# Optimization experiments

Measured on AMD Instinct MI355X. Metric: run time of the kernel, lower is better.

The kernel has to match this reference:

```python
import jax, jax.numpy as jnp
import numpy as np

D_LATENTS = 256
B, N = 8, 4096
EPS = 1e-5  # BatchNorm eps (torch default)


def _w(k, shape):
    return jax.random.normal(k, shape, jnp.float32) * 0.05


def setup_inputs() -> dict:
    key = jax.random.key(0)
    ks = jax.random.split(key, 20)
    d4, d2, d = D_LATENTS // 4, D_LATENTS // 2, D_LATENTS
    def bn(k):
        k1, k2 = jax.random.split(k)
        g = 1.0 + 0.1 * jax.random.normal(k1, (0,), jnp.float32)  # placeholder
        return g
    inp = {
        "x": jax.random.normal(ks[0], (B, 3, N), jnp.float32),
        "conv1_w": _w(ks[1], (d4, 3)),
        "bn1_g": 1.0 + 0.1 * jax.random.normal(ks[2], (d4,), jnp.float32),
        "bn1_b": 0.1 * jax.random.normal(ks[3], (d4,), jnp.float32),
        "conv2_w": _w(ks[4], (d4, d4)),
        "bn2_g": 1.0 + 0.1 * jax.random.normal(ks[5], (d4,), jnp.float32),
        "bn2_b": 0.1 * jax.random.normal(ks[6], (d4,), jnp.float32),
        "le0_w1": _w(ks[7], (d2, d2)),
        "le0_g1": 1.0 + 0.1 * jax.random.normal(ks[8], (d2,), jnp.float32),
        "le0_b1": 0.1 * jax.random.normal(ks[9], (d2,), jnp.float32),
        "le0_w2": _w(ks[10], (d2, d2)),
        "le0_g2": 1.0 + 0.1 * jax.random.normal(ks[11], (d2,), jnp.float32),
        "le0_b2": 0.1 * jax.random.normal(ks[12], (d2,), jnp.float32),
        "le1_w1": _w(ks[13], (d, d)),
        "le1_g1": 1.0 + 0.1 * jax.random.normal(ks[14], (d,), jnp.float32),
        "le1_b1": 0.1 * jax.random.normal(ks[15], (d,), jnp.float32),
        "le1_w2": _w(ks[16], (d, d)),
        "le1_g2": 1.0 + 0.1 * jax.random.normal(ks[17], (d,), jnp.float32),
        "le1_b2": 0.1 * jax.random.normal(ks[18], (d,), jnp.float32),
    }
    return inp


def _bn_relu(y, g, b, axes, ch_axis):
    # BatchNorm (training-mode batch stats, biased var like torch) + ReLU
    m = jnp.mean(y, axes, keepdims=True)
    v = jnp.var(y, axes, keepdims=True)
    shp = [1] * y.ndim
    shp[ch_axis] = -1
    return jax.nn.relu((y - m) * jax.lax.rsqrt(v + EPS) * g.reshape(shp) + b.reshape(shp))


def _square_distance(src, dst):
    # src [B,S,3], dst [B,N,3] -> [B,S,N]
    return (jnp.sum(src * src, -1, keepdims=True)
            - 2.0 * jnp.einsum('bsc,bnc->bsn', src, dst)
            + jnp.sum(dst * dst, -1)[:, None, :])


def _fps(xyz, npoint):
    # farthest point sampling, deterministic start at index 0
    Bb, Nn, _ = xyz.shape
    def step(carry, _):
        dist_min, farthest = carry
        centroid = jnp.take_along_axis(xyz, farthest[:, None, None], axis=1)  # [B,1,3]
        d = jnp.sum((xyz - centroid) ** 2, -1)  # [B,N]
        dist_min = jnp.minimum(dist_min, d)
        nxt = jnp.argmax(dist_min, -1).astype(jnp.int32)
        return (dist_min, nxt), farthest
    init = (jnp.full((Bb, Nn), 1e10, xyz.dtype), jnp.zeros((Bb,), jnp.int32))
    _, idxs = jax.lax.scan(step, init, None, length=npoint)
    return jnp.transpose(idxs)  # [B, npoint]


def _sample_and_group(npoint, nsample, xyz, points):
    # PCT-style: FPS centers, kNN neighbors (radius unused), concat(rel, center)
    Bb = xyz.shape[0]
    fps_idx = _fps(xyz, npoint)                       # [B,S]
    bidx = jnp.arange(Bb)[:, None]
    new_xyz = xyz[bidx, fps_idx]                      # [B,S,3]
    new_pts = points[bidx, fps_idx]                   # [B,S,D]
    d2 = _square_distance(new_xyz, xyz)               # [B,S,N]
    _, knn_idx = jax.lax.top_k(-d2, nsample)          # [B,S,ns]
    grouped = points[jnp.arange(Bb)[:, None, None], knn_idx]  # [B,S,ns,D]
    center = new_pts[:, :, None, :]
    feat = jnp.concatenate([grouped - center,
                            jnp.broadcast_to(center, grouped.shape)], axis=-1)
    return new_xyz, feat  # [B,S,3], [B,S,ns,2D]


def _local_encoder(x4, w1, g1, b1, w2, g2, b2):
    # x4: [b,n,s,d] -> conv1x1/bn/relu x2 over channel dim, max over s -> [b,out,n]
    y = jnp.einsum('bnsd,od->bnos', x4, w1)
    y = _bn_relu(y, g1, b1, (0, 1, 3), 2)
    y = jnp.einsum('bnis,oi->bnos', y, w2)
    y = _bn_relu(y, g2, b2, (0, 1, 3), 2)
    y = jnp.max(y, axis=3)                # [b,n,out]
    return jnp.transpose(y, (0, 2, 1))    # [b,out,n]


def reference(x, conv1_w, bn1_g, bn1_b, conv2_w, bn2_g, bn2_b,
              le0_w1, le0_g1, le0_b1, le0_w2, le0_g2, le0_b2,
              le1_w1, le1_g1, le1_b1, le1_w2, le1_g2, le1_b2):
    xyz = jnp.transpose(x, (0, 2, 1))                 # [B,N,3]
    y = jnp.einsum('bcn,oc->bon', x, conv1_w)
    y = _bn_relu(y, bn1_g, bn1_b, (0, 2), 1)
    y = jnp.einsum('bcn,oc->bon', y, conv2_w)
    y = _bn_relu(y, bn2_g, bn2_b, (0, 2), 1)
    pts = jnp.transpose(y, (0, 2, 1))                 # [B,N,d4]
    new_xyz, feat = _sample_and_group(512, 32, xyz, pts)       # [B,512,32,d2]
    f0 = _local_encoder(feat, le0_w1, le0_g1, le0_b1, le0_w2, le0_g2, le0_b2)  # [B,d2,512]
    pts1 = jnp.transpose(f0, (0, 2, 1))
    _, feat2 = _sample_and_group(256, 32, new_xyz, pts1)       # [B,256,32,d]
    f1 = _local_encoder(feat2, le1_w1, le1_g1, le1_b1, le1_w2, le1_g2, le1_b2)  # [B,d,256]
    return f1
```

## Files before the change

kernel.cpp:

```cpp
#include <hip/hip_runtime.h>

constexpr int B_  = 8;
constexpr int N_  = 4096;
constexpr int NP1 = 512;
constexpr int NP2 = 256;
constexpr float EPS_ = 1e-5f;

typedef __attribute__((ext_vector_type(8))) short bhalf8;
typedef __attribute__((ext_vector_type(4))) float f32x4;

__device__ inline short f2bf(float f) {
  union { float fv; unsigned u; } v; v.fv = f;
  unsigned r = v.u + 0x7FFFu + ((v.u >> 16) & 1u);
  return (short)(r >> 16);
}

template<int CTRL>
__device__ inline void dpp_amax(unsigned &khi, unsigned &klo) {
  unsigned ohi = (unsigned)__builtin_amdgcn_mov_dpp((int)khi, CTRL, 0xF, 0xF, false);
  unsigned olo = (unsigned)__builtin_amdgcn_mov_dpp((int)klo, CTRL, 0xF, 0xF, false);
  if (ohi > khi || (ohi == khi && olo > klo)) { khi = ohi; klo = olo; }
}
__device__ inline void swz16_amax(unsigned &khi, unsigned &klo) {
  unsigned ohi = (unsigned)__builtin_amdgcn_ds_swizzle((int)khi, 0x401F);
  unsigned olo = (unsigned)__builtin_amdgcn_ds_swizzle((int)klo, 0x401F);
  if (ohi > khi || (ohi == khi && olo > klo)) { khi = ohi; klo = olo; }
}
__device__ inline void x32_amax(unsigned &khi, unsigned &klo) {
  unsigned ohi = (unsigned)__shfl_xor((int)khi, 32);
  unsigned olo = (unsigned)__shfl_xor((int)klo, 32);
  if (ohi > khi || (ohi == khi && olo > klo)) { khi = ohi; klo = olo; }
}
__device__ inline unsigned ford(float f) {
  unsigned u = __float_as_uint(f);
  return u ^ (((unsigned)((int)u >> 31)) | 0x80000000u);
}

constexpr int S_BN1 = 0;
constexpr int S_BN2 = 128;
constexpr int S_L0A = 256;
constexpr int S_L0B = 512;
constexpr int S_L1A = 768;
constexpr int S_L1B = 1280;
constexpr int S_TOTAL = 1792;

constexpr size_t OFF_T1   = 0;
constexpr size_t OFF_YBUF = OFF_T1   + 2097152;
constexpr size_t OFF_PTS1 = OFF_YBUF + 16777216;
constexpr size_t OFF_NXYZ = OFF_PTS1 + 524288;
constexpr size_t OFF_WT2C = OFF_NXYZ + 12288;
constexpr size_t OFF_BW0A = OFF_WT2C + 4096;
constexpr size_t OFF_BW0B = OFF_BW0A + 8192;
constexpr size_t OFF_BW1A = OFF_BW0B + 8192;
constexpr size_t OFF_BW1B = OFF_BW1A + 32768;
constexpr size_t OFF_STAT = OFF_BW1B + 32768;
constexpr size_t OFF_INT  = OFF_STAT + 1792;

__global__ void prep_kernel(const float* __restrict__ conv2w,
                            const float* __restrict__ w0a, const float* __restrict__ w0b,
                            const float* __restrict__ w1a, const float* __restrict__ w1b,
                            float* __restrict__ wt2c,
                            short* __restrict__ b0a, short* __restrict__ b0b,
                            short* __restrict__ b1a, short* __restrict__ b1b) {
  int idx = blockIdx.x * 256 + threadIdx.x;
  if (idx < 4096) { int d = idx >> 6, o = idx & 63; wt2c[idx] = conv2w[o*64 + d]; return; }
  idx -= 4096;
  const float* w; short* dst; int D;
  if      (idx <  2048) { w = w0a; dst = b0a; D = 128; }
  else if (idx <  4096) { w = w0b; dst = b0b; D = 128; idx -= 2048; }
  else if (idx < 12288) { w = w1a; dst = b1a; D = 256; idx -= 4096; }
  else if (idx < 20480) { w = w1b; dst = b1b; D = 256; idx -= 12288; }
  else return;
  int kblk = idx / D, o = idx % D;
  const float* src = w + (size_t)o*D + kblk*8;
  bhalf8 pk;
#pragma unroll
  for (int j = 0; j < 8; ++j) pk[j] = f2bf(src[j]);
  *(bhalf8*)&dst[(size_t)idx*8] = pk;
}

__global__ __launch_bounds__(256) void conv1_kernel(
    const float* __restrict__ x, const float* __restrict__ w,
    float* __restrict__ t1, float* __restrict__ stats) {
  __shared__ float xs[3][64];
  __shared__ float redS[4][64], redQ[4][64];
  int blk = blockIdx.x;
  int b = blk >> 6, n0 = (blk & 63) << 6;
  int t = threadIdx.x;
  if (t < 192) { int c = t >> 6, nl = t & 63; xs[c][nl] = x[((size_t)b*3 + c)*N_ + n0 + nl]; }
  __syncthreads();
  int o = t & 63, ng = t >> 6;
  float w0 = w[o*3+0], w1 = w[o*3+1], w2 = w[o*3+2];
  float ls = 0.f, lq = 0.f;
#pragma unroll
  for (int k = 0; k < 16; ++k) {
    int nl = ng*16 + k;
    float y = xs[0][nl]*w0 + xs[1][nl]*w1 + xs[2][nl]*w2;
    t1[((size_t)b*N_ + n0 + nl)*64 + o] = y;
    ls += y; lq += y*y;
  }
  redS[ng][o] = ls; redQ[ng][o] = lq;
  __syncthreads();
  if (t < 64) {
    float s = redS[0][t]+redS[1][t]+redS[2][t]+redS[3][t];
    float q = redQ[0][t]+redQ[1][t]+redQ[2][t]+redQ[3][t];
    atomicAdd(&stats[S_BN1 + t], s);
    atomicAdd(&stats[S_BN1 + 64 + t], q);
  }
}

__global__ __launch_bounds__(256) void conv2_kernel(
    const float* __restrict__ t1, const float* __restrict__ g1, const float* __restrict__ b1,
    const float* __restrict__ wt2c, float* __restrict__ t2, float* __restrict__ stats) {
  constexpr int P = 68;
  __shared__ float at[64*P];
  __shared__ float sc[64], sh[64];
  __shared__ float redS[4][64], redQ[4][64];
  int blk = blockIdx.x;
  int b = blk >> 6, n0 = (blk & 63) << 6;
  int t = threadIdx.x;
  if (t < 64) {
    float m = stats[S_BN1 + t] * (1.f/32768.f);
    float v = stats[S_BN1 + 64 + t] * (1.f/32768.f) - m*m;
    float s = g1[t] * rsqrtf(v + EPS_);
    sc[t] = s; sh[t] = b1[t] - m*s;
  }
  __syncthreads();
  for (int e = t; e < 4096; e += 256) {
    int nl = e >> 6, c = e & 63;
    float v = t1[((size_t)b*N_ + n0 + nl)*64 + c];
    at[c*P + nl] = fmaxf(v*sc[c] + sh[c], 0.f);
  }
  __syncthreads();
  int o = t & 63, ng = t >> 6;
  float acc[16];
#pragma unroll
  for (int k = 0; k < 16; ++k) acc[k] = 0.f;
  for (int i = 0; i < 64; ++i) {
    float wv = wt2c[i*64 + o];
    const float* ar = &at[i*P + ng*16];
#pragma unroll
    for (int k = 0; k < 16; k += 4) {
      float4 a4 = *(const float4*)(ar + k);
      acc[k+0] += a4.x*wv; acc[k+1] += a4.y*wv;
      acc[k+2] += a4.z*wv; acc[k+3] += a4.w*wv;
    }
  }
  float ls = 0.f, lq = 0.f;
#pragma unroll
  for (int k = 0; k < 16; ++k) {
    float y = acc[k];
    t2[((size_t)b*N_ + n0 + ng*16 + k)*64 + o] = y;
    ls += y; lq += y*y;
  }
  redS[ng][o] = ls; redQ[ng][o] = lq;
  __syncthreads();
  if (t < 64) {
    float s = redS[0][t]+redS[1][t]+redS[2][t]+redS[3][t];
    float q = redQ[0][t]+redQ[1][t]+redQ[2][t]+redQ[3][t];
    atomicAdd(&stats[S_BN2 + t], s);
    atomicAdd(&stats[S_BN2 + 64 + t], q);
  }
}

__global__ __launch_bounds__(256) void bn2fin_kernel(
    const float* __restrict__ t2, const float* __restrict__ g2, const float* __restrict__ b2,
    const float* __restrict__ stats, float* __restrict__ pts) {
  int idx = blockIdx.x*256 + threadIdx.x;
  int o = idx & 63;
  float m = stats[S_BN2 + o] * (1.f/32768.f);
  float v = stats[S_BN2 + 64 + o] * (1.f/32768.f) - m*m;
  float s = g2[o] * rsqrtf(v + EPS_);
  pts[idx] = fmaxf(t2[idx]*s + (b2[o] - m*s), 0.f);
}

template<int NPTS, int NSEL1, int NSEL2, int NT>
__global__ __launch_bounds__(NT) void fps_fused_kernel(
    const float* __restrict__ x,
    int* __restrict__ sel1, float* __restrict__ nxyz, int* __restrict__ sel2) {
  constexpr int K  = NPTS / NT;
  constexpr int NS = NT / 32;
  __shared__ float lx[NPTS], ly[NPTS], lz[NPTS];
  __shared__ float sx[NSEL1], sy[NSEL1], sz[NSEL1];
  __shared__ unsigned long long wk[2][NS];
  __shared__ int seli1[NSEL1];
  __shared__ int seli2[NSEL2];
  int b = blockIdx.x, t = threadIdx.x;
  int lane = t & 63, wid = t >> 6;
  const float* cb = x + (size_t)b * 3 * NPTS;
  for (int i = t; i < NPTS; i += NT) {
    lx[i] = cb[i]; ly[i] = cb[NPTS + i]; lz[i] = cb[2*NPTS + i];
  }
  __syncthreads();
  float px[K], py[K], pz[K], dm[K];
#pragma unroll
  for (int k = 0; k < K; ++k) {
    int p = t + k*NT;
    px[k] = lx[p]; py[k] = ly[p]; pz[k] = lz[p];
    dm[k] = 1e10f;
  }
  float cx = lx[0], cy = ly[0], cz = lz[0];
  if (t == 0) { seli1[0] = 0; sx[0] = cx; sy[0] = cy; sz[0] = cz; }
  for (int it = 1; it < NSEL1; ++it) {
    float bv = -1.f; int bi = 0;
#pragma unroll
    for (int k = 0; k < K; ++k) {
      float dx = px[k]-cx, dy = py[k]-cy, dz = pz[k]-cz;
      float d = dx*dx + dy*dy + dz*dz;
      float nd = fminf(dm[k], d);
      dm[k] = nd;
      if (nd > bv) { bv = nd; bi = t + k*NT; }
    }
    unsigned khi = __float_as_uint(bv), klo = ~(unsigned)bi;
    dpp_amax<0xB1>(khi, klo);
    dpp_amax<0x4E>(khi, klo);
    dpp_amax<0x141>(khi, klo);
    dpp_amax<0x140>(khi, klo);
    swz16_amax(khi, klo);
    int p = it & 1;
    if ((lane & 31) == 0)
      wk[p][wid*2 + (lane >> 5)] = ((unsigned long long)khi << 32) | klo;
    __syncthreads();
    unsigned long long best = wk[p][0];
#pragma unroll
    for (int i2 = 1; i2 < NS; ++i2) { unsigned long long v2 = wk[p][i2]; if (v2 > best) best = v2; }
    int Bi = (int)(~(unsigned)best);
    cx = lx[Bi]; cy = ly[Bi]; cz = lz[Bi];
    if (t == 0) { seli1[it] = Bi; sx[it] = cx; sy[it] = cy; sz[it] = cz; }
  }
  __syncthreads();
  if (t < 64) {
    constexpr int K2 = NSEL1 / 64;
    float qx[K2], qy[K2], qz[K2], dm2[K2];
#pragma unroll
    for (int k = 0; k < K2; ++k) {
      int p = t + k*64;
      qx[k] = sx[p]; qy[k] = sy[p]; qz[k] = sz[p];
      dm2[k] = 1e10f;
    }
    cx = sx[0]; cy = sy[0]; cz = sz[0];
    if (t == 0) seli2[0] = 0;
    for (int it = 1; it < NSEL2; ++it) {
      float bv = -1.f; int bi = 0;
#pragma unroll
      for (int k = 0; k < K2; ++k) {
        float dx = qx[k]-cx, dy = qy[k]-cy, dz = qz[k]-cz;
        float d = dx*dx + dy*dy + dz*dz;
        float nd = fminf(dm2[k], d);
        dm2[k] = nd;
        if (nd > bv) { bv = nd; bi = t + k*64; }
      }
      unsigned khi = __float_as_uint(bv), klo = ~(unsigned)bi;
      dpp_amax<0xB1>(khi, klo);
      dpp_amax<0x4E>(khi, klo);
      dpp_amax<0x141>(khi, klo);
      dpp_amax<0x140>(khi, klo);
      swz16_amax(khi, klo);
      x32_amax(khi, klo);
      int Bi = (int)~klo;
      cx = sx[Bi]; cy = sy[Bi]; cz = sz[Bi];
      if (t == 0) seli2[it] = Bi;
    }
  } else {
    for (int i = t - 64; i < NSEL1; i += NT - 64) {
      sel1[(size_t)b*NSEL1 + i] = seli1[i];
      float* q = nxyz + ((size_t)b*NSEL1 + i)*3;
      q[0] = sx[i]; q[1] = sy[i]; q[2] = sz[i];
    }
  }
  __syncthreads();
  for (int i = t; i < NSEL2; i += NT) sel2[(size_t)b*NSEL2 + i] = seli2[i];
}

template<int NDST, int NQ, int NT, bool XLAY>
__global__ __launch_bounds__(NT) void knn_kernel(
    const float* __restrict__ dst, const float* __restrict__ nxyz,
    const int* __restrict__ qmap, int* __restrict__ knn_out) {
  constexpr int K  = NDST / NT;
  constexpr int NS = NT / 32;
  __shared__ unsigned long long wk[2][NS];
  __shared__ int kos[32];
  int blk = blockIdx.x, t = threadIdx.x;
  int b = blk / NQ, q = blk % NQ;
  int qrow = b*NP1 + (qmap ? qmap[b*NQ + q] : q);
  float qx = nxyz[qrow*3+0], qy = nxyz[qrow*3+1], qz = nxyz[qrow*3+2];
  float q2 = (qx*qx + qy*qy) + qz*qz;
  const float* db = dst + (size_t)b * (XLAY ? 3*NDST : NDST*3);
  float d2r[K];
#pragma unroll
  for (int k = 0; k < K; ++k) {
    int j = t + k*NT;
    float xx, yy, zz;
    if (XLAY) { xx = db[j]; yy = db[NDST + j]; zz = db[2*NDST + j]; }
    else      { xx = db[j*3]; yy = db[j*3+1]; zz = db[j*3+2]; }
    float dot = (qx*xx + qy*yy) + qz*zz;
    float p2  = (xx*xx + yy*yy) + zz*zz;
    d2r[k] = (q2 - 2.f*dot) + p2;
  }
  for (int r = 0; r < 32; ++r) {
    float bv = 3e38f; int bi = t;
#pragma unroll
    for (int k = 0; k < K; ++k) {
      float v = d2r[k];
      if (v < bv) { bv = v; bi = t + k*NT; }
    }
    unsigned khi = ~ford(bv), klo = ~(unsigned)bi;
    dpp_amax<0xB1>(khi, klo);
    dpp_amax<0x4E>(khi, klo);
    dpp_amax<0x141>(khi, klo);
    dpp_amax<0x140>(khi, klo);
    swz16_amax(khi, klo);
    int p = r & 1;
    if ((t & 31) == 0)
      wk[p][t >> 5] = ((unsigned long long)khi << 32) | klo;
    __syncthreads();
    unsigned long long best = wk[p][0];
#pragma unroll
    for (int i2 = 1; i2 < NS; ++i2) { unsigned long long v2 = wk[p][i2]; if (v2 > best) best = v2; }
    int Bi = (int)(~(unsigned)best);
    if (t == 0) kos[r] = Bi;
#pragma unroll
    for (int k = 0; k < K; ++k)
      if (t + k*NT == Bi) d2r[k] = 3e38f;
  }
  __syncthreads();
  if (t < 32) knn_out[((size_t)b*NQ + q)*32 + t] = kos[t];
}

template<int D, int PW, int NP, int SRCN, int SOFF>
__global__ __launch_bounds__(256) void gemm1_kernel(
    const float* __restrict__ pts, const int* __restrict__ knn,
    const int* __restrict__ cent, const short* __restrict__ bw,
    float* __restrict__ ybuf, float* __restrict__ stats) {
  constexpr int KB = D/8;
  __shared__ __align__(16) short As[64*D];
  __shared__ float cen_s[2*PW];
  __shared__ int kid_s[64];
  __shared__ float sstat[2*D];
  int t = threadIdx.x, blk = blockIdx.x;
  int g0 = blk*2;
  if (t < 64) {
    int grp = t >> 5, s = t & 31;
    kid_s[t] = knn[((size_t)(g0+grp))*32 + s];
  }
  for (int i = t; i < 2*PW; i += 256) {
    int grp = i / PW, d = i % PW;
    int g = g0 + grp; int b = g / NP; int ci = cent[g];
    cen_s[i] = pts[((size_t)b*SRCN + ci)*PW + d];
  }
  for (int i = t; i < 2*D; i += 256) sstat[i] = 0.f;
  __syncthreads();
  for (int task = t; task < 64*KB; task += 256) {
    int row = task / KB, c = task % KB;
    int grp = row >> 5;
    int g = g0 + grp; int b = g / NP;
    int d = c*8;
    float v0,v1,v2,v3,v4,v5,v6,v7;
    if (d < PW) {
      const float* src = pts + ((size_t)b*SRCN + kid_s[row])*PW + d;
      float4 x0 = *(const float4*)src, x1 = *(const float4*)(src+4);
      const float* cc = &cen_s[grp*PW + d];
      v0=x0.x-cc[0]; v1=x0.y-cc[1]; v2=x0.z-cc[2]; v3=x0.w-cc[3];
      v4=x1.x-cc[4]; v5=x1.y-cc[5]; v6=x1.z-cc[6]; v7=x1.w-cc[7];
    } else {
      const float* cc = &cen_s[grp*PW + d - PW];
      v0=cc[0]; v1=cc[1]; v2=cc[2]; v3=cc[3]; v4=cc[4]; v5=cc[5]; v6=cc[6]; v7=cc[7];
    }
    bhalf8 pk;
    pk[0]=f2bf(v0); pk[1]=f2bf(v1); pk[2]=f2bf(v2); pk[3]=f2bf(v3);
    pk[4]=f2bf(v4); pk[5]=f2bf(v5); pk[6]=f2bf(v6); pk[7]=f2bf(v7);
    int a16 = row*KB + (c ^ (row & 7));
    *(bhalf8*)&As[a16*8] = pk;
  }
  __syncthreads();
  int w = t >> 6, l = t & 63, lr = l & 15, lg = l >> 4;
  f32x4 acc[D/16];
#pragma unroll
  for (int ct = 0; ct < D/16; ++ct) acc[ct] = (f32x4){0.f,0.f,0.f,0.f};
  int r = w*16 + lr;
#pragma unroll
  for (int kg = 0; kg < D/32; ++kg) {
    int c = (kg*4 + lg) ^ (r & 7);
    bhalf8 af = *(const bhalf8*)&As[(r*KB + c)*8];
#pragma unroll
    for (int ct = 0; ct < D/16; ++ct) {
      bhalf8 bf = *(const bhalf8*)&bw[((size_t)(kg*4 + lg)*D + ct*16 + lr)*8];
      acc[ct] = __builtin_amdgcn_mfma_f32_16x16x32_bf16(af, bf, acc[ct], 0, 0, 0);
    }
  }
  size_t rb = (size_t)blk*64 + w*16 + lg*4;
#pragma unroll
  for (int ct = 0; ct < D/16; ++ct) {
    int col = ct*16 + lr;
    f32x4 a = acc[ct];
    float* yp = ybuf + rb*D + col;
    yp[0] = a[0]; yp[(size_t)D] = a[1]; yp[(size_t)2*D] = a[2]; yp[(size_t)3*D] = a[3];
    float s = a[0]+a[1]+a[2]+a[3];
    float q = a[0]*a[0]+a[1]*a[1]+a[2]*a[2]+a[3]*a[3];
    s += __shfl_xor(s, 16); q += __shfl_xor(q, 16);
    s += __shfl_xor(s, 32); q += __shfl_xor(q, 32);
    if (lg == 0) { atomicAdd(&sstat[col], s); atomicAdd(&sstat[D+col], q); }
  }
  __syncthreads();
  for (int i = t; i < 2*D; i += 256) atomicAdd(&stats[SOFF+i], sstat[i]);
}

template<int D, int SIN, int SOUT, int CNT>
__global__ __launch_bounds__(256) void gemm2_kernel(
    const float* __restrict__ g1, const float* __restrict__ b1,
    const short* __restrict__ bw, const float* __restrict__ ybuf,
    float* __restrict__ mm, float* __restrict__ stats) {
  __shared__ __align__(16) float scsh[2*D];
  __shared__ float sstat[2*D];
  __shared__ float wmax[4][D], wmin[4][D];
  int t = threadIdx.x, blk = blockIdx.x;
  for (int i = t; i < D; i += 256) {
    float m = stats[SIN + i] * (1.f/(float)CNT);
    float v = stats[SIN + D + i] * (1.f/(float)CNT) - m*m;
    float s = g1[i] * rsqrtf(v + EPS_);
    scsh[i] = s; scsh[D+i] = b1[i] - m*s;
  }
  for (int i = t; i < 2*D; i += 256) sstat[i] = 0.f;
  __syncthreads();
  int w = t >> 6, l = t & 63, lr = l & 15, lg = l >> 4;
  size_t row = (size_t)blk*64 + w*16 + lr;
  const float* yrow = ybuf + row*D;
  f32x4 acc[D/16];
#pragma unroll
  for (int ct = 0; ct < D/16; ++ct) acc[ct] = (f32x4){0.f,0.f,0.f,0.f};
#pragma unroll
  for (int kg = 0; kg < D/32; ++kg) {
    int k = kg*32 + lg*8;
    float4 y0 = *(const float4*)(yrow + k);
    float4 y1 = *(const float4*)(yrow + k + 4);
    bhalf8 af;
    af[0] = f2bf(fmaxf(y0.x*scsh[k+0] + scsh[D+k+0], 0.f));
    af[1] = f2bf(fmaxf(y0.y*scsh[k+1] + scsh[D+k+1], 0.f));
    af[2] = f2bf(fmaxf(y0.z*scsh[k+2] + scsh[D+k+2], 0.f));
    af[3] = f2bf(fmaxf(y0.w*scsh[k+3] + scsh[D+k+3], 0.f));
    af[4] = f2bf(fmaxf(y1.x*scsh[k+4] + scsh[D+k+4], 0.f));
    af[5] = f2bf(fmaxf(y1.y*scsh[k+5] + scsh[D+k+5], 0.f));
    af[6] = f2bf(fmaxf(y1.z*scsh[k+6] + scsh[D+k+6], 0.f));
    af[7] = f2bf(fmaxf(y1.w*scsh[k+7] + scsh[D+k+7], 0.f));
#pragma unroll
    for (int ct = 0; ct < D/16; ++ct) {
      bhalf8 bf = *(const bhalf8*)&bw[((size_t)(kg*4 + lg)*D + ct*16 + lr)*8];
      acc[ct] = __builtin_amdgcn_mfma_f32_16x16x32_bf16(af, bf, acc[ct], 0, 0, 0);
    }
  }
#pragma unroll
  for (int ct = 0; ct < D/16; ++ct) {
    int col = ct*16 + lr;
    f32x4 a = acc[ct];
    float mx = fmaxf(fmaxf(a[0], a[1]), fmaxf(a[2], a[3]));
    float mn = fminf(fminf(a[0], a[1]), fminf(a[2], a[3]));
    mx = fmaxf(mx, __shfl_xor(mx, 16)); mn = fminf(mn, __shfl_xor(mn, 16));
    mx = fmaxf(mx, __shfl_xor(mx, 32)); mn = fminf(mn, __shfl_xor(mn, 32));
    if (lg == 0) { wmax[w][col] = mx; wmin[w][col] = mn; }
    float s = a[0]+a[1]+a[2]+a[3];
    float q = a[0]*a[0]+a[1]*a[1]+a[2]*a[2]+a[3]*a[3];
    s += __shfl_xor(s, 16); q += __shfl_xor(q, 16);
    s += __shfl_xor(s, 32); q += __shfl_xor(q, 32);
    if (lg == 0) { atomicAdd(&sstat[col], s); atomicAdd(&sstat[D+col], q); }
  }
  __syncthreads();
  for (int i = t; i < 2*D; i += 256) {
    int g = i / D, col = i - g*D;
    float mx = fmaxf(wmax[2*g][col], wmax[2*g+1][col]);
    float mn = fminf(wmin[2*g][col], wmin[2*g+1][col]);
    float* mp = mm + ((size_t)blk*2 + g)*2*D;
    mp[col] = mx; mp[D + col] = mn;
    atomicAdd(&stats[SOUT+i], sstat[i]);
  }
}

template<int D, int NP, int SOFF, int CNT, bool TR>
__global__ __launch_bounds__(256) void le3_kernel(
    const float* __restrict__ g2, const float* __restrict__ b2,
    const float* __restrict__ mm, const float* __restrict__ stats,
    float* __restrict__ out) {
  int idx = blockIdx.x*256 + threadIdx.x;
  int g = idx / D, o = idx - g*D;
  float m = stats[SOFF + o] * (1.f/(float)CNT);
  float v = stats[SOFF + D + o] * (1.f/(float)CNT) - m*m;
  float s = g2[o] * rsqrtf(v + EPS_);
  float sh = b2[o] - m*s;
  const float* mp = mm + (size_t)g*2*D;
  float pick = (s >= 0.f) ? mp[o] : mp[D + o];
  float r = fmaxf(pick*s + sh, 0.f);
  if (TR) { int b = g / NP, n = g - b*NP; out[((size_t)b*D + o)*NP + n] = r; }
  else    out[(size_t)g*D + o] = r;
}

extern "C" void kernel_launch(void* const* d_in, const int* in_sizes, int n_in,
                              void* d_out, int out_size, void* d_ws, size_t ws_size,
                              hipStream_t stream) {
  (void)in_sizes; (void)n_in; (void)out_size; (void)ws_size;
  const float* x       = (const float*)d_in[0];
  const float* conv1_w = (const float*)d_in[1];
  const float* bn1_g   = (const float*)d_in[2];
  const float* bn1_b   = (const float*)d_in[3];
  const float* conv2_w = (const float*)d_in[4];
  const float* bn2_g   = (const float*)d_in[5];
  const float* bn2_b   = (const float*)d_in[6];
  const float* le0_w1  = (const float*)d_in[7];
  const float* le0_g1  = (const float*)d_in[8];
  const float* le0_b1  = (const float*)d_in[9];
  const float* le0_w2  = (const float*)d_in[10];
  const float* le0_g2  = (const float*)d_in[11];
  const float* le0_b2  = (const float*)d_in[12];
  const float* le1_w1  = (const float*)d_in[13];
  const float* le1_g1  = (const float*)d_in[14];
  const float* le1_b1  = (const float*)d_in[15];
  const float* le1_w2  = (const float*)d_in[16];
  const float* le1_g2  = (const float*)d_in[17];
  const float* le1_b2  = (const float*)d_in[18];

  float* ws   = (float*)d_ws;
  float* t1   = ws + OFF_T1;
  float* ybuf = ws + OFF_YBUF;
  float* t2   = ybuf;
  float* mm   = t1;
  float* pts1 = ws + OFF_PTS1;
  float* nxyz = ws + OFF_NXYZ;
  float* wt2c = ws + OFF_WT2C;
  short* bw0a = (short*)(ws + OFF_BW0A);
  short* bw0b = (short*)(ws + OFF_BW0B);
  short* bw1a = (short*)(ws + OFF_BW1A);
  short* bw1b = (short*)(ws + OFF_BW1B);
  float* stats = ws + OFF_STAT;
  int* fps1 = (int*)(ws + OFF_INT);
  int* fps2 = fps1 + 4096;
  int* knn1 = fps2 + 2048;
  int* knn2 = knn1 + 131072;

  hipMemsetAsync(stats, 0, S_TOTAL*sizeof(float), stream);
  prep_kernel<<<96, 256, 0, stream>>>(conv2_w, le0_w1, le0_w2, le1_w1, le1_w2,
                                      wt2c, bw0a, bw0b, bw1a, bw1b);
  conv1_kernel<<<512, 256, 0, stream>>>(x, conv1_w, t1, stats);
  conv2_kernel<<<512, 256, 0, stream>>>(t1, bn1_g, bn1_b, wt2c, t2, stats);
  bn2fin_kernel<<<8192, 256, 0, stream>>>(t2, bn2_g, bn2_b, stats, t1);

  fps_fused_kernel<4096, 512, 256, 256><<<8, 256, 0, stream>>>(x, fps1, nxyz, fps2);
  knn_kernel<4096, 512, 256, true ><<<4096, 256, 0, stream>>>(x, nxyz, nullptr, knn1);
  knn_kernel< 512, 256, 256, false><<<2048, 256, 0, stream>>>(nxyz, nxyz, fps2, knn2);

  gemm1_kernel<128,  64, 512, 4096, S_L0A><<<2048, 256, 0, stream>>>(t1, knn1, fps1, bw0a, ybuf, stats);
  gemm2_kernel<128, S_L0A, S_L0B, 131072><<<2048, 256, 0, stream>>>(le0_g1, le0_b1, bw0b, ybuf, mm, stats);
  le3_kernel<128, 512, S_L0B, 131072, false><<<2048, 256, 0, stream>>>(le0_g2, le0_b2, mm, stats, pts1);

  gemm1_kernel<256, 128, 256,  512, S_L1A><<<1024, 256, 0, stream>>>(pts1, knn2, fps2, bw1a, ybuf, stats);
  gemm2_kernel<256, S_L1A, S_L1B, 65536><<<1024, 256, 0, stream>>>(le1_g1, le1_b1, bw1b, ybuf, mm, stats);
  le3_kernel<256, 256, S_L1B, 65536, true><<<2048, 256, 0, stream>>>(le1_g2, le1_b2, mm, stats, (float*)d_out);
}
```

Measured before the change: 1.020 ms.

## Fuse weight prep, conv/BN front end and FPS into one persistent kernel

Weight preparation, conv1, conv2, the BN2 finalize and farthest point sampling become a single launch of 264 blocks. The first 8 blocks run FPS, one per batch. The other 256 blocks process the conv tiles and sync between the BN stages with atomic-counter grid barriers. This removes four kernel launches and lets the serial FPS work run alongside the conv/BN pipeline instead of after it. In exchange it depends on all blocks being co-resident for the spin barriers, and it makes every block reserve the larger FPS shared-memory footprint.

After: 973.0 us. 1.05x faster.

```diff
diff --git a/kernel.cpp b/kernel.cpp
--- a/kernel.cpp
+++ b/kernel.cpp
@@ -54,23 +54,22 @@
 constexpr size_t OFF_BW1A = OFF_BW0B + 8192;
 constexpr size_t OFF_BW1B = OFF_BW1A + 32768;
 constexpr size_t OFF_STAT = OFF_BW1B + 32768;
-constexpr size_t OFF_INT  = OFF_STAT + 1792;
-
-__global__ void prep_kernel(const float* __restrict__ conv2w,
-                            const float* __restrict__ w0a, const float* __restrict__ w0b,
-                            const float* __restrict__ w1a, const float* __restrict__ w1b,
-                            float* __restrict__ wt2c,
-                            short* __restrict__ b0a, short* __restrict__ b0b,
-                            short* __restrict__ b1a, short* __restrict__ b1b) {
-  int idx = blockIdx.x * 256 + threadIdx.x;
+constexpr size_t OFF_CNT  = OFF_STAT + S_TOTAL;
+constexpr size_t OFF_INT  = OFF_CNT + 16;
+
+__device__ inline void prep_elem(int idx, const float* __restrict__ conv2w,
+                                 const float* __restrict__ w0a, const float* __restrict__ w0b,
+                                 const float* __restrict__ w1a, const float* __restrict__ w1b,
+                                 float* __restrict__ wt2c,
+                                 short* __restrict__ b0a, short* __restrict__ b0b,
+                                 short* __restrict__ b1a, short* __restrict__ b1b) {
   if (idx < 4096) { int d = idx >> 6, o = idx & 63; wt2c[idx] = conv2w[o*64 + d]; return; }
   idx -= 4096;
   const float* w; short* dst; int D;
   if      (idx <  2048) { w = w0a; dst = b0a; D = 128; }
   else if (idx <  4096) { w = w0b; dst = b0b; D = 128; idx -= 2048; }
   else if (idx < 12288) { w = w1a; dst = b1a; D = 256; idx -= 4096; }
-  else if (idx < 20480) { w = w1b; dst = b1b; D = 256; idx -= 12288; }
-  else return;
+  else                  { w = w1b; dst = b1b; D = 256; idx -= 12288; }
   int kblk = idx / D, o = idx % D;
   const float* src = w + (size_t)o*D + kblk*8;
   bhalf8 pk;
@@ -79,176 +78,63 @@
   *(bhalf8*)&dst[(size_t)idx*8] = pk;
 }
 
-__global__ __launch_bounds__(256) void conv1_kernel(
-    const float* __restrict__ x, const float* __restrict__ w,
-    float* __restrict__ t1, float* __restrict__ stats) {
-  __shared__ float xs[3][64];
-  __shared__ float redS[4][64], redQ[4][64];
-  int blk = blockIdx.x;
-  int b = blk >> 6, n0 = (blk & 63) << 6;
+struct FpsSmem {
+  float lx[4096], ly[4096], lz[4096];
+  float sx[512], sy[512], sz[512];
+  unsigned long long wk[2][8];
+  int seli1[512];
+  int seli2[256];
+};
+struct ConvSmem {
+  float xs[3][64];
+  float redS[4][64], redQ[4][64];
+  float sc[64], sh[64];
+  float at[64*68];
+};
+
+__global__ __launch_bounds__(256) void front_kernel(
+    const float* __restrict__ x,
+    const float* __restrict__ conv1w, const float* __restrict__ bn1g, const float* __restrict__ bn1b,
+    const float* __restrict__ conv2w, const float* __restrict__ bn2g, const float* __restrict__ bn2b,
+    const float* __restrict__ w0a, const float* __restrict__ w0b,
+    const float* __restrict__ w1a, const float* __restrict__ w1b,
+    float* __restrict__ wt2c,
+    short* __restrict__ b0a, short* __restrict__ b0b,
+    short* __restrict__ b1a, short* __restrict__ b1b,
+    float* __restrict__ t1, float* __restrict__ t2,
+    float* __restrict__ stats, int* __restrict__ cnt,
+    int* __restrict__ sel1, float* __restrict__ nxyz, int* __restrict__ sel2) {
+  __shared__ __align__(16) char smem_raw[sizeof(FpsSmem)];
   int t = threadIdx.x;
-  if (t < 192) { int c = t >> 6, nl = t & 63; xs[c][nl] = x[((size_t)b*3 + c)*N_ + n0 + nl]; }
-  __syncthreads();
-  int o = t & 63, ng = t >> 6;
-  float w0 = w[o*3+0], w1 = w[o*3+1], w2 = w[o*3+2];
-  float ls = 0.f, lq = 0.f;
-#pragma unroll
-  for (int k = 0; k < 16; ++k) {
-    int nl = ng*16 + k;
-    float y = xs[0][nl]*w0 + xs[1][nl]*w1 + xs[2][nl]*w2;
-    t1[((size_t)b*N_ + n0 + nl)*64 + o] = y;
-    ls += y; lq += y*y;
-  }
-  redS[ng][o] = ls; redQ[ng][o] = lq;
-  __syncthreads();
-  if (t < 64) {
-    float s = redS[0][t]+redS[1][t]+redS[2][t]+redS[3][t];
-    float q = redQ[0][t]+redQ[1][t]+redQ[2][t]+redQ[3][t];
-    atomicAdd(&stats[S_BN1 + t], s);
-    atomicAdd(&stats[S_BN1 + 64 + t], q);
-  }
-}
-
-__global__ __launch_bounds__(256) void conv2_kernel(
-    const float* __restrict__ t1, const float* __restrict__ g1, const float* __restrict__ b1,
-    const float* __restrict__ wt2c, float* __restrict__ t2, float* __restrict__ stats) {
-  constexpr int P = 68;
-  __shared__ float at[64*P];
-  __shared__ float sc[64], sh[64];
-  __shared__ float redS[4][64], redQ[4][64];
-  int blk = blockIdx.x;
-  int b = blk >> 6, n0 = (blk & 63) << 6;
-  int t = threadIdx.x;
-  if (t < 64) {
-    float m = stats[S_BN1 + t] * (1.f/32768.f);
-    float v = stats[S_BN1 + 64 + t] * (1.f/32768.f) - m*m;
-    float s = g1[t] * rsqrtf(v + EPS_);
-    sc[t] = s; sh[t] = b1[t] - m*s;
-  }
-  __syncthreads();
-  for (int e = t; e < 4096; e += 256) {
-    int nl = e >> 6, c = e & 63;
-    float v = t1[((size_t)b*N_ + n0 + nl)*64 + c];
-    at[c*P + nl] = fmaxf(v*sc[c] + sh[c], 0.f);
-  }
-  __syncthreads();
-  int o = t & 63, ng = t >> 6;
-  float acc[16];
-#pragma unroll
-  for (int k = 0; k < 16; ++k) acc[k] = 0.f;
-  for (int i = 0; i < 64; ++i) {
-    float wv = wt2c[i*64 + o];
-    const float* ar = &at[i*P + ng*16];
-#pragma unroll
-    for (int k = 0; k < 16; k += 4) {
-      float4 a4 = *(const float4*)(ar + k);
-      acc[k+0] += a4.x*wv; acc[k+1] += a4.y*wv;
-      acc[k+2] += a4.z*wv; acc[k+3] += a4.w*wv;
-    }
-  }
-  float ls = 0.f, lq = 0.f;
-#pragma unroll
-  for (int k = 0; k < 16; ++k) {
-    float y = acc[k];
-    t2[((size_t)b*N_ + n0 + ng*16 + k)*64 + o] = y;
-    ls += y; lq += y*y;
-  }
-  redS[ng][o] = ls; redQ[ng][o] = lq;
-  __syncthreads();
-  if (t < 64) {
-    float s = redS[0][t]+redS[1][t]+redS[2][t]+redS[3][t];
-    float q = redQ[0][t]+redQ[1][t]+redQ[2][t]+redQ[3][t];
-    atomicAdd(&stats[S_BN2 + t], s);
-    atomicAdd(&stats[S_BN2 + 64 + t], q);
-  }
-}
-
-__global__ __launch_bounds__(256) void bn2fin_kernel(
-    const float* __restrict__ t2, const float* __restrict__ g2, const float* __restrict__ b2,
-    const float* __restrict__ stats, float* __restrict__ pts) {
-  int idx = blockIdx.x*256 + threadIdx.x;
-  int o = idx & 63;
-  float m = stats[S_BN2 + o] * (1.f/32768.f);
-  float v = stats[S_BN2 + 64 + o] * (1.f/32768.f) - m*m;
-  float s = g2[o] * rsqrtf(v + EPS_);
-  pts[idx] = fmaxf(t2[idx]*s + (b2[o] - m*s), 0.f);
-}
-
-template<int NPTS, int NSEL1, int NSEL2, int NT>
-__global__ __launch_bounds__(NT) void fps_fused_kernel(
-    const float* __restrict__ x,
-    int* __restrict__ sel1, float* __restrict__ nxyz, int* __restrict__ sel2) {
-  constexpr int K  = NPTS / NT;
-  constexpr int NS = NT / 32;
-  __shared__ float lx[NPTS], ly[NPTS], lz[NPTS];
-  __shared__ float sx[NSEL1], sy[NSEL1], sz[NSEL1];
-  __shared__ unsigned long long wk[2][NS];
-  __shared__ int seli1[NSEL1];
-  __shared__ int seli2[NSEL2];
-  int b = blockIdx.x, t = threadIdx.x;
-  int lane = t & 63, wid = t >> 6;
-  const float* cb = x + (size_t)b * 3 * NPTS;
-  for (int i = t; i < NPTS; i += NT) {
-    lx[i] = cb[i]; ly[i] = cb[NPTS + i]; lz[i] = cb[2*NPTS + i];
-  }
-  __syncthreads();
-  float px[K], py[K], pz[K], dm[K];
-#pragma unroll
-  for (int k = 0; k < K; ++k) {
-    int p = t + k*NT;
-    px[k] = lx[p]; py[k] = ly[p]; pz[k] = lz[p];
-    dm[k] = 1e10f;
-  }
-  float cx = lx[0], cy = ly[0], cz = lz[0];
-  if (t == 0) { seli1[0] = 0; sx[0] = cx; sy[0] = cy; sz[0] = cz; }
-  for (int it = 1; it < NSEL1; ++it) {
-    float bv = -1.f; int bi = 0;
+  if (blockIdx.x < 8) {
+    constexpr int NPTS = 4096, NSEL1 = 512, NSEL2 = 256, NT = 256;
+    constexpr int K = NPTS / NT, NS = NT / 32;
+    FpsSmem& S = *reinterpret_cast<FpsSmem*>(smem_raw);
+    int b = blockIdx.x;
+    int lane = t & 63, wid = t >> 6;
+    const float* cb = x + (size_t)b * 3 * NPTS;
+    for (int i = t; i < NPTS; i += NT) {
+      S.lx[i] = cb[i]; S.ly[i] = cb[NPTS + i]; S.lz[i] = cb[2*NPTS + i];
+    }
+    __syncthreads();
+    float px[K], py[K], pz[K], dm[K];
 #pragma unroll
     for (int k = 0; k < K; ++k) {
-      float dx = px[k]-cx, dy = py[k]-cy, dz = pz[k]-cz;
-      float d = dx*dx + dy*dy + dz*dz;
-      float nd = fminf(dm[k], d);
-      dm[k] = nd;
-      if (nd > bv) { bv = nd; bi = t + k*NT; }
-    }
-    unsigned khi = __float_as_uint(bv), klo = ~(unsigned)bi;
-    dpp_amax<0xB1>(khi, klo);
-    dpp_amax<0x4E>(khi, klo);
-    dpp_amax<0x141>(khi, klo);
-    dpp_amax<0x140>(khi, klo);
-    swz16_amax(khi, klo);
-    int p = it & 1;
-    if ((lane & 31) == 0)
-      wk[p][wid*2 + (lane >> 5)] = ((unsigned long long)khi << 32) | klo;
-    __syncthreads();
-    unsigned long long best = wk[p][0];
-#pragma unroll
-    for (int i2 = 1; i2 < NS; ++i2) { unsigned long long v2 = wk[p][i2]; if (v2 > best) best = v2; }
-    int Bi = (int)(~(unsigned)best);
-    cx = lx[Bi]; cy = ly[Bi]; cz = lz[Bi];
-    if (t == 0) { seli1[it] = Bi; sx[it] = cx; sy[it] = cy; sz[it] = cz; }
-  }
-  __syncthreads();
-  if (t < 64) {
-    constexpr int K2 = NSEL1 / 64;
-    float qx[K2], qy[K2], qz[K2], dm2[K2];
-#pragma unroll
-    for (int k = 0; k < K2; ++k) {
-      int p = t + k*64;
-      qx[k] = sx[p]; qy[k] = sy[p]; qz[k] = sz[p];
-      dm2[k] = 1e10f;
-    }
-    cx = sx[0]; cy = sy[0]; cz = sz[0];
-    if (t == 0) seli2[0] = 0;
-    for (int it = 1; it < NSEL2; ++it) {
+      int p = t + k*NT;
+      px[k] = S.lx[p]; py[k] = S.ly[p]; pz[k] = S.lz[p];
+      dm[k] = 1e10f;
+    }
+    float cx = S.lx[0], cy = S.ly[0], cz = S.lz[0];
+    if (t == 0) { S.seli1[0] = 0; S.sx[0] = cx; S.sy[0] = cy; S.sz[0] = cz; }
+    for (int it = 1; it < NSEL1; ++it) {
       float bv = -1.f; int bi = 0;
 #pragma unroll
-      for (int k = 0; k < K2; ++k) {
-        float dx = qx[k]-cx, dy = qy[k]-cy, dz = qz[k]-cz;
+      for (int k = 0; k < K; ++k) {
+        float dx = px[k]-cx, dy = py[k]-cy, dz = pz[k]-cz;
         float d = dx*dx + dy*dy + dz*dz;
-        float nd = fminf(dm2[k], d);
-        dm2[k] = nd;
-        if (nd > bv) { bv = nd; bi = t + k*64; }
+        float nd = fminf(dm[k], d);
+        dm[k] = nd;
+        if (nd > bv) { bv = nd; bi = t + k*NT; }
       }
       unsigned khi = __float_as_uint(bv), klo = ~(unsigned)bi;
       dpp_amax<0xB1>(khi, klo);
@@ -256,20 +142,165 @@
       dpp_amax<0x141>(khi, klo);
       dpp_amax<0x140>(khi, klo);
       swz16_amax(khi, klo);
-      x32_amax(khi, klo);
-      int Bi = (int)~klo;
-      cx = sx[Bi]; cy = sy[Bi]; cz = sz[Bi];
-      if (t == 0) seli2[it] = Bi;
-    }
-  } else {
-    for (int i = t - 64; i < NSEL1; i += NT - 64) {
-      sel1[(size_t)b*NSEL1 + i] = seli1[i];
-      float* q = nxyz + ((size_t)b*NSEL1 + i)*3;
-      q[0] = sx[i]; q[1] = sy[i]; q[2] = sz[i];
-    }
-  }
-  __syncthreads();
-  for (int i = t; i < NSEL2; i += NT) sel2[(size_t)b*NSEL2 + i] = seli2[i];
+      int p = it & 1;
+      if ((lane & 31) == 0)
+        S.wk[p][wid*2 + (lane >> 5)] = ((unsigned long long)khi << 32) | klo;
+      __syncthreads();
+      unsigned long long best = S.wk[p][0];
+#pragma unroll
+      for (int i2 = 1; i2 < NS; ++i2) { unsigned long long v2 = S.wk[p][i2]; if (v2 > best) best = v2; }
+      int Bi = (int)(~(unsigned)best);
+      cx = S.lx[Bi]; cy = S.ly[Bi]; cz = S.lz[Bi];
+      if (t == 0) { S.seli1[it] = Bi; S.sx[it] = cx; S.sy[it] = cy; S.sz[it] = cz; }
+    }
+    __syncthreads();
+    if (t < 64) {
+      constexpr int K2 = NSEL1 / 64;
+      float qx[K2], qy[K2], qz[K2], dm2[K2];
+#pragma unroll
+      for (int k = 0; k < K2; ++k) {
+        int p = t + k*64;
+        qx[k] = S.sx[p]; qy[k] = S.sy[p]; qz[k] = S.sz[p];
+        dm2[k] = 1e10f;
+      }
+      cx = S.sx[0]; cy = S.sy[0]; cz = S.sz[0];
+      if (t == 0) S.seli2[0] = 0;
+      for (int it = 1; it < NSEL2; ++it) {
+        float bv = -1.f; int bi = 0;
+#pragma unroll
+        for (int k = 0; k < K2; ++k) {
+          float dx = qx[k]-cx, dy = qy[k]-cy, dz = qz[k]-cz;
+          float d = dx*dx + dy*dy + dz*dz;
+          float nd = fminf(dm2[k], d);
+          dm2[k] = nd;
+          if (nd > bv) { bv = nd; bi = t + k*64; }
+        }
+        unsigned khi = __float_as_uint(bv), klo = ~(unsigned)bi;
+        dpp_amax<0xB1>(khi, klo);
+        dpp_amax<0x4E>(khi, klo);
+        dpp_amax<0x141>(khi, klo);
+        dpp_amax<0x140>(khi, klo);
+        swz16_amax(khi, klo);
+        x32_amax(khi, klo);
+        int Bi = (int)~klo;
+        cx = S.sx[Bi]; cy = S.sy[Bi]; cz = S.sz[Bi];
+        if (t == 0) S.seli2[it] = Bi;
+      }
+    } else {
+      for (int i = t - 64; i < NSEL1; i += NT - 64) {
+        sel1[(size_t)b*NSEL1 + i] = S.seli1[i];
+        float* q = nxyz + ((size_t)b*NSEL1 + i)*3;
+        q[0] = S.sx[i]; q[1] = S.sy[i]; q[2] = S.sz[i];
+      }
+    }
+    __syncthreads();
+    for (int i = t; i < NSEL2; i += NT) sel2[(size_t)b*NSEL2 + i] = S.seli2[i];
+    return;
+  }
+  ConvSmem& C = *reinterpret_cast<ConvSmem*>(smem_raw);
+  int cb = blockIdx.x - 8;
+  { int idx = cb*256 + t;
+    if (idx < 24576) prep_elem(idx, conv2w, w0a, w0b, w1a, w1b, wt2c, b0a, b0b, b1a, b1b); }
+  for (int tile = cb; tile < 512; tile += 256) {
+    int b = tile >> 6, n0 = (tile & 63) << 6;
+    if (t < 192) { int c = t >> 6, nl = t & 63; C.xs[c][nl] = x[((size_t)b*3 + c)*N_ + n0 + nl]; }
+    __syncthreads();
+    int o = t & 63, ng = t >> 6;
+    float w0 = conv1w[o*3+0], w1 = conv1w[o*3+1], w2 = conv1w[o*3+2];
+    float ls = 0.f, lq = 0.f;
+#pragma unroll
+    for (int k = 0; k < 16; ++k) {
+      int nl = ng*16 + k;
+      float y = C.xs[0][nl]*w0 + C.xs[1][nl]*w1 + C.xs[2][nl]*w2;
+      t1[((size_t)b*N_ + n0 + nl)*64 + o] = y;
+      ls += y; lq += y*y;
+    }
+    C.redS[ng][o] = ls; C.redQ[ng][o] = lq;
+    __syncthreads();
+    if (t < 64) {
+      float s = C.redS[0][t]+C.redS[1][t]+C.redS[2][t]+C.redS[3][t];
+      float q = C.redQ[0][t]+C.redQ[1][t]+C.redQ[2][t]+C.redQ[3][t];
+      atomicAdd(&stats[S_BN1 + t], s);
+      atomicAdd(&stats[S_BN1 + 64 + t], q);
+    }
+    __syncthreads();
+  }
+  if (t == 0) {
+    __threadfence();
+    __hip_atomic_fetch_add(&cnt[0], 1, __ATOMIC_ACQ_REL, __HIP_MEMORY_SCOPE_AGENT);
+    while (__hip_atomic_load(&cnt[0], __ATOMIC_ACQUIRE, __HIP_MEMORY_SCOPE_AGENT) < 256)
+      __builtin_amdgcn_s_sleep(8);
+    __threadfence();
+  }
+  __syncthreads();
+  if (t < 64) {
+    float m = stats[S_BN1 + t] * (1.f/32768.f);
+    float v = stats[S_BN1 + 64 + t] * (1.f/32768.f) - m*m;
+    float s = bn1g[t] * rsqrtf(v + EPS_);
+    C.sc[t] = s; C.sh[t] = bn1b[t] - m*s;
+  }
+  __syncthreads();
+  for (int tile = cb; tile < 512; tile += 256) {
+    int b = tile >> 6, n0 = (tile & 63) << 6;
+    constexpr int P = 68;
+    for (int e = t; e < 4096; e += 256) {
+      int nl = e >> 6, c = e & 63;
+      float v = t1[((size_t)b*N_ + n0 + nl)*64 + c];
+      C.at[c*P + nl] = fmaxf(v*C.sc[c] + C.sh[c], 0.f);
+    }
+    __syncthreads();
+    int o = t & 63, ng = t >> 6;
+    float acc[16];
+#pragma unroll
+    for (int k = 0; k < 16; ++k) acc[k] = 0.f;
+    for (int i = 0; i < 64; ++i) {
+      float wv = wt2c[i*64 + o];
+      const float* ar = &C.at[i*P + ng*16];
+#pragma unroll
+      for (int k = 0; k < 16; k += 4) {
+        float4 a4 = *(const float4*)(ar + k);
+        acc[k+0] += a4.x*wv; acc[k+1] += a4.y*wv;
+        acc[k+2] += a4.z*wv; acc[k+3] += a4.w*wv;
+      }
+    }
+    float ls = 0.f, lq = 0.f;
+#pragma unroll
+    for (int k = 0; k < 16; ++k) {
+      float y = acc[k];
+      t2[((size_t)b*N_ + n0 + ng*16 + k)*64 + o] = y;
+      ls += y; lq += y*y;
+    }
+    C.redS[ng][o] = ls; C.redQ[ng][o] = lq;
+    __syncthreads();
+    if (t < 64) {
+      float s = C.redS[0][t]+C.redS[1][t]+C.redS[2][t]+C.redS[3][t];
+      float q = C.redQ[0][t]+C.redQ[1][t]+C.redQ[2][t]+C.redQ[3][t];
+      atomicAdd(&stats[S_BN2 + t], s);
+      atomicAdd(&stats[S_BN2 + 64 + t], q);
+    }
+    __syncthreads();
+  }
+  if (t == 0) {
+    __threadfence();
+    __hip_atomic_fetch_add(&cnt[1], 1, __ATOMIC_ACQ_REL, __HIP_MEMORY_SCOPE_AGENT);
+    while (__hip_atomic_load(&cnt[1], __ATOMIC_ACQUIRE, __HIP_MEMORY_SCOPE_AGENT) < 256)
+      __builtin_amdgcn_s_sleep(8);
+    __threadfence();
+  }
+  __syncthreads();
+  {
+    int o = t & 63;
+    float m = stats[S_BN2 + o] * (1.f/32768.f);
+    float v = stats[S_BN2 + 64 + o] * (1.f/32768.f) - m*m;
+    float s = bn2g[o] * rsqrtf(v + EPS_);
+    float sh = bn2b[o] - m*s;
+    for (int tile = cb; tile < 512; tile += 256)
+#pragma unroll
+      for (int j = 0; j < 16; ++j) {
+        size_t idx = (size_t)tile*4096 + j*256 + t;
+        t1[idx] = fmaxf(t2[idx]*s + sh, 0.f);
+      }
+  }
 }
 
 template<int NDST, int NQ, int NT, bool XLAY>
@@ -529,19 +560,19 @@
   short* bw1a = (short*)(ws + OFF_BW1A);
   short* bw1b = (short*)(ws + OFF_BW1B);
   float* stats = ws + OFF_STAT;
+  int*   cnt   = (int*)(ws + OFF_CNT);
   int* fps1 = (int*)(ws + OFF_INT);
   int* fps2 = fps1 + 4096;
   int* knn1 = fps2 + 2048;
   int* knn2 = knn1 + 131072;
 
-  hipMemsetAsync(stats, 0, S_TOTAL*sizeof(float), stream);
-  prep_kernel<<<96, 256, 0, stream>>>(conv2_w, le0_w1, le0_w2, le1_w1, le1_w2,
-                                      wt2c, bw0a, bw0b, bw1a, bw1b);
-  conv1_kernel<<<512, 256, 0, stream>>>(x, conv1_w, t1, stats);
-  conv2_kernel<<<512, 256, 0, stream>>>(t1, bn1_g, bn1_b, wt2c, t2, stats);
-  bn2fin_kernel<<<8192, 256, 0, stream>>>(t2, bn2_g, bn2_b, stats, t1);
-
-  fps_fused_kernel<4096, 512, 256, 256><<<8, 256, 0, stream>>>(x, fps1, nxyz, fps2);
+  hipMemsetAsync(stats, 0, (S_TOTAL + 16)*sizeof(float), stream);
+  front_kernel<<<264, 256, 0, stream>>>(x,
+      conv1_w, bn1_g, bn1_b, conv2_w, bn2_g, bn2_b,
+      le0_w1, le0_w2, le1_w1, le1_w2,
+      wt2c, bw0a, bw0b, bw1a, bw1b,
+      t1, t2, stats, cnt, fps1, nxyz, fps2);
+
   knn_kernel<4096, 512, 256, true ><<<4096, 256, 0, stream>>>(x, nxyz, nullptr, knn1);
   knn_kernel< 512, 256, 256, false><<<2048, 256, 0, stream>>>(nxyz, nxyz, fps2, knn2);
 
```
